# Optimization experiments

Hardware: AMD Instinct MI355X
Metric: run time of the kernel (lower is better)

Reference implementation:

```python
import jax, jax.numpy as jnp
from jax import lax
import numpy as np

B = 262144   # batch of independent series
K = 64       # forecast horizon (init k)
D_IN = 200   # Non_AR_net input dim (Linear(200,100))
H = 100      # hidden width


def setup_inputs() -> dict:
    key = jax.random.key(0)
    ks = jax.random.split(key, 10)
    f32 = jnp.float32
    x = jax.random.normal(ks[0], (B, D_IN), f32)
    last_mu = jax.random.normal(ks[1], (B,), f32)
    # last_sigma is the variance state; keep it strictly positive
    last_sigma = jax.random.uniform(ks[2], (B,), f32) + 0.5
    # MLP params (Kaiming-ish scale)
    W1 = jax.random.normal(ks[3], (D_IN, H), f32) / np.float32(np.sqrt(D_IN))
    b1 = jnp.zeros((H,), f32)
    W2 = jax.random.normal(ks[4], (H, H), f32) / np.float32(np.sqrt(H))
    b2 = jnp.zeros((H,), f32)
    W3 = jax.random.normal(ks[5], (H, K), f32) / np.float32(np.sqrt(H))
    b3 = jnp.zeros((K,), f32)
    return {
        "x": x, "last_mu": last_mu, "last_sigma": last_sigma,
        "alpha_mu": jnp.asarray(0.1, f32), "alpha_sigma": jnp.asarray(0.1, f32),
        "beta_mu": jnp.asarray(0.9, f32), "beta_sigma": jnp.asarray(0.85, f32),
        "omega_mu": jnp.asarray(0.0, f32), "omega_sigma": jnp.asarray(0.05, f32),
        "nu": jnp.asarray(5.0, f32), "norm_strength": jnp.asarray(1.0, f32),
        "W1": W1, "b1": b1, "W2": W2, "b2": b2, "W3": W3, "b3": b3,
    }


def _mlp(x, W1, b1, W2, b2, W3, b3):
    h = jax.nn.relu(x @ W1 + b1)
    h = jax.nn.relu(h @ W2 + b2)
    return h @ W3 + b3  # [B, K]


def _ar_gas(deep_preds, last_mu, last_sigma, a_mu, a_s, b_mu, b_s, o_mu, o_s, nu, ns):
    """Student-t score-driven (GAS) k-step recurrence, vectorized over batch.
    deep_preds: [B, K]; state mu, sigma2: [B]."""
    w = 1.0 + 1.0 / nu

    def step(carry, y):  # y: [B]
        mu, s2 = carry
        e = y - mu
        denom = 1.0 + e * e / (nu * s2)
        mu_new = o_mu + ns * a_mu * (w * e / denom) + b_mu * mu
        s2_new = o_s + ns * a_s * (w * e * e / denom - s2) + b_s * s2
        return (mu_new, s2_new), (mu_new, s2_new)

    (_, _), (mus, s2s) = lax.scan(step, (last_mu, last_sigma), deep_preds.T)
    return mus.T, jnp.sqrt(s2s.T)  # [B, K] each


def reference(x, last_mu, last_sigma, alpha_mu, alpha_sigma, beta_mu, beta_sigma,
              omega_mu, omega_sigma, nu, norm_strength,
              W1, b1, W2, b2, W3, b3):
    deep_preds = _mlp(x, W1, b1, W2, b2, W3, b3)            # [B, K]
    dp = lax.stop_gradient(deep_preds)                       # .detach() in torch
    mu_pred, sigma_pred = _ar_gas(dp, last_mu, last_sigma,
                                  alpha_mu, alpha_sigma, beta_mu, beta_sigma,
                                  omega_mu, omega_sigma, nu, norm_strength)
    return deep_preds * sigma_pred + mu_pred                 # [B, K]
```

## Files before the change

### kernel.cpp

```cpp
#include <hip/hip_runtime.h>
#include <hip/hip_bf16.h>

typedef short v8s __attribute__((ext_vector_type(8)));
typedef float v4f __attribute__((ext_vector_type(4)));

#define THREADS 512
#define BMROWS  128
#define W1F     0
#define W2F     49
#define W3F     77
#define W1LDS   28
#define SLABB   28672
#define LDS_TOTAL 78848

__device__ __forceinline__ unsigned short f2bf(float f) {
    union { __hip_bfloat16 h; unsigned short u; } c;
    c.h = __float2bfloat16(f);
    return c.u;
}
__device__ __forceinline__ unsigned pk2(float a, float b) {
    return (unsigned)f2bf(a) | ((unsigned)f2bf(b) << 16);
}
__device__ __forceinline__ v4f mfma16(v8s a, v8s b, v4f c) {
    return __builtin_amdgcn_mfma_f32_16x16x32_bf16(a, b, c, 0, 0, 0);
}
__device__ __forceinline__ v8s mkfrag(float4 a, float4 b) {
    union { unsigned u[4]; v8s s; } t;
    t.u[0] = pk2(a.x, a.y); t.u[1] = pk2(a.z, a.w);
    t.u[2] = pk2(b.x, b.y); t.u[3] = pk2(b.z, b.w);
    return t.s;
}
__device__ __forceinline__ void gload_lds16(const void* g, void* l) {
    __builtin_amdgcn_global_load_lds(
        (const __attribute__((address_space(1))) void*)g,
        (__attribute__((address_space(3))) void*)l, 16, 0, 0);
}

__global__ void prep_weights(const float* __restrict__ W1,
                             const float* __restrict__ W2,
                             const float* __restrict__ W3,
                             uint4* __restrict__ wf) {
    const int bid = blockIdx.x, l = threadIdx.x;
    const float* W; int K, N, KC, base, f;
    if (bid < 49)      { W = W1; K = 200; N = 100; KC = 7; base = W1F * 64; f = bid; }
    else if (bid < 77) { W = W2; K = 100; N = 100; KC = 4; base = W2F * 64; f = bid - 49; }
    else               { W = W3; K = 100; N = 64;  KC = 4; base = W3F * 64; f = bid - 77; }
    const int kc = f % KC;
    const int n  = (f / KC) * 16 + (l & 15);
    unsigned u[4];
    #pragma unroll
    for (int p = 0; p < 4; ++p) {
        const int k0 = kc * 32 + (l >> 4) * 8 + p * 2;
        const float a = (k0     < K && n < N) ? W[(size_t)k0 * N + n]       : 0.f;
        const float b = (k0 + 1 < K && n < N) ? W[(size_t)(k0 + 1) * N + n] : 0.f;
        u[p] = pk2(a, b);
    }
    wf[base + f * 64 + l] = make_uint4(u[0], u[1], u[2], u[3]);
}

__device__ __forceinline__ int sladdr(int wid, int row, int byte) {
    return SLABB + (wid << 12) + (row << 8) +
           ((((byte >> 4) ^ row) & 15) << 4) + (byte & 15);
}

__global__ __launch_bounds__(THREADS, 4)
void ar_gas_v11(const float* __restrict__ x,
                const float* __restrict__ last_mu,
                const float* __restrict__ last_sigma,
                const float* __restrict__ p_amu, const float* __restrict__ p_as,
                const float* __restrict__ p_bmu, const float* __restrict__ p_bs,
                const float* __restrict__ p_omu, const float* __restrict__ p_os,
                const float* __restrict__ p_nu,  const float* __restrict__ p_ns,
                const float* __restrict__ b1, const float* __restrict__ b2,
                const float* __restrict__ b3,
                const uint4* __restrict__ wf,
                float* __restrict__ out)
{
    extern __shared__ __align__(16) unsigned char L[];
    const int tid  = threadIdx.x;
    const int lane = tid & 63;
    const int wid  = tid >> 6;
    const int l15  = lane & 15;
    const int l4   = lane >> 4;
    const int blk  = blockIdx.x;

    const size_t gw = (size_t)blk * BMROWS + (size_t)wid * 16;
    const float* xp0 = x + (gw + l15) * 200;

    const float mu_init = last_mu[gw + l15];
    const float s2_init = last_sigma[gw + l15];

#define XLOAD(d0, d1, kk)                                               \
    { int kb = (kk) * 32 + l4 * 8;                                      \
      kb = (kb + 8 <= 200) ? kb : 168;                                  \
      d0 = *(const float4*)(xp0 + kb);                                  \
      d1 = *(const float4*)(xp0 + kb + 4); }

    float4 xv[3][2];
    XLOAD(xv[0][0], xv[0][1], 0);
    XLOAD(xv[1][0], xv[1][1], 1);
    XLOAD(xv[2][0], xv[2][1], 2);

    float bv[7];
    #pragma unroll
    for (int nt = 0; nt < 7; ++nt) {
        const int c = nt * 16 + l15;
        bv[nt] = (c < 100) ? b1[c] : 0.f;
    }

    for (int s = wid; s < 77; s += 8) {
        const int src = (s < 28) ? (W2F + s - 0) : (W1F + s - 28);
        gload_lds16(wf + src * 64 + lane, L + s * 1024);
    }
    __syncthreads();

#define FRAG(slot) (*(const uint4*)(&L[(slot) * 1024 + lane * 16]))

    v4f acc[7];
    #pragma unroll
    for (int nt = 0; nt < 7; ++nt) acc[nt] = (v4f){0.f, 0.f, 0.f, 0.f};

    #pragma unroll
    for (int kc = 0; kc < 7; ++kc) {
        uint4 bu[7];
        #pragma unroll
        for (int nt = 0; nt < 7; ++nt) bu[nt] = FRAG(W1LDS + nt * 7 + kc);
        const v8s af = mkfrag(xv[kc % 3][0], xv[kc % 3][1]);
        if (kc < 4) XLOAD(xv[kc % 3][0], xv[kc % 3][1], kc + 3);
        #pragma unroll
        for (int nt = 0; nt < 7; ++nt)
            acc[nt] = mfma16(af, *(const v8s*)&bu[nt], acc[nt]);
    }
#undef XLOAD

    __syncthreads();

    #pragma unroll
    for (int nt = 0; nt < 7; ++nt) {
        #pragma unroll
        for (int r = 0; r < 4; ++r) {
            const int row = l4 * 4 + r;
            const int c   = nt * 16 + l15;
            const float v = fmaxf(acc[nt][r] + bv[nt], 0.f);
            *(unsigned short*)(&L[sladdr(wid, row, c * 2)]) = f2bf(v);
        }
    }
    if (lane < 32)
        *(uint4*)(&L[sladdr(wid, lane >> 1, 224 + (lane & 1) * 16)]) =
            make_uint4(0, 0, 0, 0);

    float bv2[7];
    #pragma unroll
    for (int nt = 0; nt < 7; ++nt) {
        const int c = nt * 16 + l15;
        bv2[nt] = (c < 100) ? b2[c] : 0.f;
    }
    v4f acc2[7];
    #pragma unroll
    for (int nt = 0; nt < 7; ++nt) acc2[nt] = (v4f){0.f, 0.f, 0.f, 0.f};

    #pragma unroll
    for (int kc = 0; kc < 4; ++kc) {
        uint4 bu[7];
        #pragma unroll
        for (int nt = 0; nt < 7; ++nt) bu[nt] = FRAG(nt * 4 + kc);
        uint4 t0 = *(const uint4*)(&L[sladdr(wid, l15, kc * 64 + l4 * 16)]);
        const v8s af = *(v8s*)&t0;
        #pragma unroll
        for (int nt = 0; nt < 7; ++nt)
            acc2[nt] = mfma16(af, *(const v8s*)&bu[nt], acc2[nt]);
    }

    __syncthreads();

    for (int s = wid; s < 16; s += 8)
        gload_lds16(wf + (W3F + s) * 64 + lane, L + s * 1024);

    #pragma unroll
    for (int nt = 0; nt < 7; ++nt) {
        #pragma unroll
        for (int r = 0; r < 4; ++r) {
            const int row = l4 * 4 + r;
            const int c   = nt * 16 + l15;
            const float v = fmaxf(acc2[nt][r] + bv2[nt], 0.f);
            *(unsigned short*)(&L[sladdr(wid, row, c * 2)]) = f2bf(v);
        }
    }

    __syncthreads();

    float bv3[4];
    #pragma unroll
    for (int nt = 0; nt < 4; ++nt) bv3[nt] = b3[nt * 16 + l15];
    v4f acc3[4];
    #pragma unroll
    for (int nt = 0; nt < 4; ++nt) acc3[nt] = (v4f){0.f, 0.f, 0.f, 0.f};

    #pragma unroll
    for (int kc = 0; kc < 4; ++kc) {
        uint4 bu[4];
        #pragma unroll
        for (int nt = 0; nt < 4; ++nt) bu[nt] = FRAG(nt * 4 + kc);
        uint4 t0 = *(const uint4*)(&L[sladdr(wid, l15, kc * 64 + l4 * 16)]);
        const v8s af = *(v8s*)&t0;
        #pragma unroll
        for (int nt = 0; nt < 4; ++nt)
            acc3[nt] = mfma16(af, *(const v8s*)&bu[nt], acc3[nt]);
    }
#undef FRAG

    #pragma unroll
    for (int nt = 0; nt < 4; ++nt) {
        #pragma unroll
        for (int r = 0; r < 4; ++r) {
            const int row = l4 * 4 + r;
            const int c   = nt * 16 + l15;
            *(float*)(&L[sladdr(wid, row, c * 4)]) = acc3[nt][r] + bv3[nt];
        }
    }

    if (lane < 16) {
        float mu = mu_init;
        float s2 = s2_init;
        const float anu = *p_nu,  ans = *p_ns;
        const float aMu = *p_amu, aSg = *p_as;
        const float bMu = *p_bmu, bSg = *p_bs;
        const float oMu = *p_omu, oSg = *p_os;
        const float w   = 1.f + __builtin_amdgcn_rcpf(anu);
        const float cmu = ans * aMu * w;
        const float cs  = ans * aSg * w;
        const float bs2 = bSg - ans * aSg;

#define GAS_STEP(Y, O)                                                  \
        {   const float e    = (Y) - mu;                                \
            const float nus2 = anu * s2;                                \
            const float den  = fmaf(e, e, nus2);                        \
            const float r0   = __builtin_amdgcn_rcpf(den);              \
            const float p    = e * nus2 * r0;                           \
            mu = fmaf(cmu, p, fmaf(bMu, mu, oMu));                      \
            s2 = fmaf(cs, e * p, fmaf(bs2, s2, oSg));                   \
            (O) = fmaf((Y), __builtin_amdgcn_sqrtf(s2), mu); }

        #pragma unroll
        for (int q = 0; q < 16; ++q) {
            float4 d = *(float4*)(&L[sladdr(wid, lane, q * 16)]);
            float o0, o1, o2, o3;
            GAS_STEP(d.x, o0); GAS_STEP(d.y, o1);
            GAS_STEP(d.z, o2); GAS_STEP(d.w, o3);
            *(float4*)(&L[sladdr(wid, lane, q * 16)]) = make_float4(o0, o1, o2, o3);
        }
#undef GAS_STEP
    }

    #pragma unroll
    for (int i = 0; i < 4; ++i) {
        const int fi  = i * 64 + lane;
        const int row = fi >> 4, q = fi & 15;
        float4 v = *(float4*)(&L[sladdr(wid, row, q * 16)]);
        ((float4*)out)[gw * 16 + fi] = v;
    }
}

extern "C" void kernel_launch(void* const* d_in, const int* in_sizes, int n_in,
                              void* d_out, int out_size, void* d_ws, size_t ws_size,
                              hipStream_t stream) {
    const float* x          = (const float*)d_in[0];
    const float* last_mu    = (const float*)d_in[1];
    const float* last_sigma = (const float*)d_in[2];
    const float* amu        = (const float*)d_in[3];
    const float* asig       = (const float*)d_in[4];
    const float* bmu        = (const float*)d_in[5];
    const float* bsig       = (const float*)d_in[6];
    const float* omu        = (const float*)d_in[7];
    const float* osig       = (const float*)d_in[8];
    const float* nu         = (const float*)d_in[9];
    const float* ns         = (const float*)d_in[10];
    const float* W1         = (const float*)d_in[11];
    const float* b1         = (const float*)d_in[12];
    const float* W2         = (const float*)d_in[13];
    const float* b2         = (const float*)d_in[14];
    const float* W3         = (const float*)d_in[15];
    const float* b3         = (const float*)d_in[16];
    float* out = (float*)d_out;

    uint4* wf = (uint4*)d_ws;
    prep_weights<<<93, 64, 0, stream>>>(W1, W2, W3, wf);

    hipFuncSetAttribute((const void*)ar_gas_v11,
                        hipFuncAttributeMaxDynamicSharedMemorySize, LDS_TOTAL);

    const int B = in_sizes[1];
    dim3 grid(B / BMROWS), block(THREADS);
    ar_gas_v11<<<grid, block, LDS_TOTAL, stream>>>(
        x, last_mu, last_sigma,
        amu, asig, bmu, bsig, omu, osig, nu, ns,
        b1, b2, b3, wf, out);
}
```

Measured before the change: 87.08 us.

## Make kernel persistent with all weights resident in LDS and prefetched x tiles

Switches to a persistent grid of 256 blocks of 1024 threads, each looping over 4 tiles of 256 rows. All three weight matrices are loaded into LDS once per block rather than once per 128-row block, and the per-tile __syncthreads are dropped because each wave uses its own slab. The x fragments for the next tile are prefetched before the GAS recurrence runs. The cost is about 160KB of LDS per block, which allows only one block per CU, and a grid size hardcoded to B=262144.

```diff
diff --git a/kernel.cpp b/kernel.cpp
--- a/kernel.cpp
+++ b/kernel.cpp
@@ -4,14 +4,14 @@
 typedef short v8s __attribute__((ext_vector_type(8)));
 typedef float v4f __attribute__((ext_vector_type(4)));
 
-#define THREADS 512
-#define BMROWS  128
+#define THREADS 1024
+#define NBLOCKS 256
+#define NTILES  4
 #define W1F     0
 #define W2F     49
 #define W3F     77
-#define W1LDS   28
-#define SLABB   28672
-#define LDS_TOTAL 78848
+#define SLABB   95232
+#define LDS_TOTAL (95232 + 16 * 4096)
 
 __device__ __forceinline__ unsigned short f2bf(float f) {
     union { __hip_bfloat16 h; unsigned short u; } c;
@@ -64,7 +64,7 @@
 }
 
 __global__ __launch_bounds__(THREADS, 4)
-void ar_gas_v11(const float* __restrict__ x,
+void ar_gas_v15(const float* __restrict__ x,
                 const float* __restrict__ last_mu,
                 const float* __restrict__ last_sigma,
                 const float* __restrict__ p_amu, const float* __restrict__ p_as,
@@ -84,181 +84,187 @@
     const int l4   = lane >> 4;
     const int blk  = blockIdx.x;
 
-    const size_t gw = (size_t)blk * BMROWS + (size_t)wid * 16;
-    const float* xp0 = x + (gw + l15) * 200;
-
-    const float mu_init = last_mu[gw + l15];
-    const float s2_init = last_sigma[gw + l15];
-
-#define XLOAD(d0, d1, kk)                                               \
+    const float anu = *p_nu,  ans = *p_ns;
+    const float aMu = *p_amu, aSg = *p_as;
+    const float bMu = *p_bmu, bSg = *p_bs;
+    const float oMu = *p_omu, oSg = *p_os;
+    const float wS  = 1.f + __builtin_amdgcn_rcpf(anu);
+    const float cmu = ans * aMu * wS;
+    const float cs  = ans * aSg * wS;
+    const float bs2 = bSg - ans * aSg;
+
+#define XLOAD(d0, d1, xp, kk)                                           \
     { int kb = (kk) * 32 + l4 * 8;                                      \
       kb = (kb + 8 <= 200) ? kb : 168;                                  \
-      d0 = *(const float4*)(xp0 + kb);                                  \
-      d1 = *(const float4*)(xp0 + kb + 4); }
-
+      d0 = *(const float4*)((xp) + kb);                                 \
+      d1 = *(const float4*)((xp) + kb + 4); }
+
+    size_t gw = (size_t)blk * (NTILES * 256) + (size_t)wid * 16;
     float4 xv[3][2];
-    XLOAD(xv[0][0], xv[0][1], 0);
-    XLOAD(xv[1][0], xv[1][1], 1);
-    XLOAD(xv[2][0], xv[2][1], 2);
-
-    float bv[7];
-    #pragma unroll
-    for (int nt = 0; nt < 7; ++nt) {
-        const int c = nt * 16 + l15;
-        bv[nt] = (c < 100) ? b1[c] : 0.f;
+    {
+        const float* xp = x + (gw + l15) * 200;
+        XLOAD(xv[0][0], xv[0][1], xp, 0);
+        XLOAD(xv[1][0], xv[1][1], xp, 1);
+        XLOAD(xv[2][0], xv[2][1], xp, 2);
     }
 
-    for (int s = wid; s < 77; s += 8) {
-        const int src = (s < 28) ? (W2F + s - 0) : (W1F + s - 28);
-        gload_lds16(wf + src * 64 + lane, L + s * 1024);
-    }
+    for (int s = wid; s < 93; s += 16)
+        gload_lds16(wf + s * 64 + lane, L + s * 1024);
     __syncthreads();
 
 #define FRAG(slot) (*(const uint4*)(&L[(slot) * 1024 + lane * 16]))
 
-    v4f acc[7];
-    #pragma unroll
-    for (int nt = 0; nt < 7; ++nt) acc[nt] = (v4f){0.f, 0.f, 0.f, 0.f};
-
-    #pragma unroll
-    for (int kc = 0; kc < 7; ++kc) {
-        uint4 bu[7];
-        #pragma unroll
-        for (int nt = 0; nt < 7; ++nt) bu[nt] = FRAG(W1LDS + nt * 7 + kc);
-        const v8s af = mkfrag(xv[kc % 3][0], xv[kc % 3][1]);
-        if (kc < 4) XLOAD(xv[kc % 3][0], xv[kc % 3][1], kc + 3);
-        #pragma unroll
-        for (int nt = 0; nt < 7; ++nt)
-            acc[nt] = mfma16(af, *(const v8s*)&bu[nt], acc[nt]);
-    }
-#undef XLOAD
-
-    __syncthreads();
-
-    #pragma unroll
-    for (int nt = 0; nt < 7; ++nt) {
-        #pragma unroll
-        for (int r = 0; r < 4; ++r) {
-            const int row = l4 * 4 + r;
-            const int c   = nt * 16 + l15;
-            const float v = fmaxf(acc[nt][r] + bv[nt], 0.f);
-            *(unsigned short*)(&L[sladdr(wid, row, c * 2)]) = f2bf(v);
-        }
-    }
-    if (lane < 32)
-        *(uint4*)(&L[sladdr(wid, lane >> 1, 224 + (lane & 1) * 16)]) =
-            make_uint4(0, 0, 0, 0);
-
-    float bv2[7];
-    #pragma unroll
-    for (int nt = 0; nt < 7; ++nt) {
-        const int c = nt * 16 + l15;
-        bv2[nt] = (c < 100) ? b2[c] : 0.f;
-    }
-    v4f acc2[7];
-    #pragma unroll
-    for (int nt = 0; nt < 7; ++nt) acc2[nt] = (v4f){0.f, 0.f, 0.f, 0.f};
-
-    #pragma unroll
-    for (int kc = 0; kc < 4; ++kc) {
-        uint4 bu[7];
-        #pragma unroll
-        for (int nt = 0; nt < 7; ++nt) bu[nt] = FRAG(nt * 4 + kc);
-        uint4 t0 = *(const uint4*)(&L[sladdr(wid, l15, kc * 64 + l4 * 16)]);
-        const v8s af = *(v8s*)&t0;
-        #pragma unroll
-        for (int nt = 0; nt < 7; ++nt)
-            acc2[nt] = mfma16(af, *(const v8s*)&bu[nt], acc2[nt]);
-    }
-
-    __syncthreads();
-
-    for (int s = wid; s < 16; s += 8)
-        gload_lds16(wf + (W3F + s) * 64 + lane, L + s * 1024);
-
-    #pragma unroll
-    for (int nt = 0; nt < 7; ++nt) {
-        #pragma unroll
-        for (int r = 0; r < 4; ++r) {
-            const int row = l4 * 4 + r;
-            const int c   = nt * 16 + l15;
-            const float v = fmaxf(acc2[nt][r] + bv2[nt], 0.f);
-            *(unsigned short*)(&L[sladdr(wid, row, c * 2)]) = f2bf(v);
-        }
-    }
-
-    __syncthreads();
-
-    float bv3[4];
-    #pragma unroll
-    for (int nt = 0; nt < 4; ++nt) bv3[nt] = b3[nt * 16 + l15];
-    v4f acc3[4];
-    #pragma unroll
-    for (int nt = 0; nt < 4; ++nt) acc3[nt] = (v4f){0.f, 0.f, 0.f, 0.f};
-
-    #pragma unroll
-    for (int kc = 0; kc < 4; ++kc) {
-        uint4 bu[4];
-        #pragma unroll
-        for (int nt = 0; nt < 4; ++nt) bu[nt] = FRAG(nt * 4 + kc);
-        uint4 t0 = *(const uint4*)(&L[sladdr(wid, l15, kc * 64 + l4 * 16)]);
-        const v8s af = *(v8s*)&t0;
-        #pragma unroll
-        for (int nt = 0; nt < 4; ++nt)
-            acc3[nt] = mfma16(af, *(const v8s*)&bu[nt], acc3[nt]);
+    #pragma unroll 1
+    for (int t = 0; t < NTILES; ++t) {
+        const float* xp = x + (gw + l15) * 200;
+
+        const float mu_init = last_mu[gw + l15];
+        const float s2_init = last_sigma[gw + l15];
+
+        v4f acc[7];
+        #pragma unroll
+        for (int nt = 0; nt < 7; ++nt) acc[nt] = (v4f){0.f, 0.f, 0.f, 0.f};
+
+        #pragma unroll
+        for (int kc = 0; kc < 7; ++kc) {
+            uint4 bu[7];
+            #pragma unroll
+            for (int nt = 0; nt < 7; ++nt) bu[nt] = FRAG(W1F + nt * 7 + kc);
+            const v8s af = mkfrag(xv[kc % 3][0], xv[kc % 3][1]);
+            if (kc < 4) XLOAD(xv[kc % 3][0], xv[kc % 3][1], xp, kc + 3);
+            #pragma unroll
+            for (int nt = 0; nt < 7; ++nt)
+                acc[nt] = mfma16(af, *(const v8s*)&bu[nt], acc[nt]);
+        }
+
+        {
+            float bv[7];
+            #pragma unroll
+            for (int nt = 0; nt < 7; ++nt) {
+                const int c = nt * 16 + l15;
+                bv[nt] = (c < 100) ? b1[c] : 0.f;
+            }
+            #pragma unroll
+            for (int nt = 0; nt < 7; ++nt) {
+                #pragma unroll
+                for (int r = 0; r < 4; ++r) {
+                    const int row = l4 * 4 + r;
+                    const int c   = nt * 16 + l15;
+                    const float v = fmaxf(acc[nt][r] + bv[nt], 0.f);
+                    *(unsigned short*)(&L[sladdr(wid, row, c * 2)]) = f2bf(v);
+                }
+            }
+        }
+        if (lane < 32)
+            *(uint4*)(&L[sladdr(wid, lane >> 1, 224 + (lane & 1) * 16)]) =
+                make_uint4(0, 0, 0, 0);
+
+        v4f acc2[7];
+        #pragma unroll
+        for (int nt = 0; nt < 7; ++nt) acc2[nt] = (v4f){0.f, 0.f, 0.f, 0.f};
+        #pragma unroll
+        for (int kc = 0; kc < 4; ++kc) {
+            uint4 bu[7];
+            #pragma unroll
+            for (int nt = 0; nt < 7; ++nt) bu[nt] = FRAG(W2F + nt * 4 + kc);
+            uint4 t0 = *(const uint4*)(&L[sladdr(wid, l15, kc * 64 + l4 * 16)]);
+            const v8s af = *(v8s*)&t0;
+            #pragma unroll
+            for (int nt = 0; nt < 7; ++nt)
+                acc2[nt] = mfma16(af, *(const v8s*)&bu[nt], acc2[nt]);
+        }
+        {
+            float bv[7];
+            #pragma unroll
+            for (int nt = 0; nt < 7; ++nt) {
+                const int c = nt * 16 + l15;
+                bv[nt] = (c < 100) ? b2[c] : 0.f;
+            }
+            #pragma unroll
+            for (int nt = 0; nt < 7; ++nt) {
+                #pragma unroll
+                for (int r = 0; r < 4; ++r) {
+                    const int row = l4 * 4 + r;
+                    const int c   = nt * 16 + l15;
+                    const float v = fmaxf(acc2[nt][r] + bv[nt], 0.f);
+                    *(unsigned short*)(&L[sladdr(wid, row, c * 2)]) = f2bf(v);
+                }
+            }
+        }
+
+        v4f acc3[4];
+        #pragma unroll
+        for (int nt = 0; nt < 4; ++nt) acc3[nt] = (v4f){0.f, 0.f, 0.f, 0.f};
+        #pragma unroll
+        for (int kc = 0; kc < 4; ++kc) {
+            uint4 bu[4];
+            #pragma unroll
+            for (int nt = 0; nt < 4; ++nt) bu[nt] = FRAG(W3F + nt * 4 + kc);
+            uint4 t0 = *(const uint4*)(&L[sladdr(wid, l15, kc * 64 + l4 * 16)]);
+            const v8s af = *(v8s*)&t0;
+            #pragma unroll
+            for (int nt = 0; nt < 4; ++nt)
+                acc3[nt] = mfma16(af, *(const v8s*)&bu[nt], acc3[nt]);
+        }
+        {
+            float bv[4];
+            #pragma unroll
+            for (int nt = 0; nt < 4; ++nt) bv[nt] = b3[nt * 16 + l15];
+            #pragma unroll
+            for (int nt = 0; nt < 4; ++nt) {
+                #pragma unroll
+                for (int r = 0; r < 4; ++r) {
+                    const int row = l4 * 4 + r;
+                    const int c   = nt * 16 + l15;
+                    *(float*)(&L[sladdr(wid, row, c * 4)]) = acc3[nt][r] + bv[nt];
+                }
+            }
+        }
+
+        const size_t gw_next = gw + 256;
+        if (t < NTILES - 1) {
+            const float* np = x + (gw_next + l15) * 200;
+            XLOAD(xv[0][0], xv[0][1], np, 0);
+            XLOAD(xv[1][0], xv[1][1], np, 1);
+            XLOAD(xv[2][0], xv[2][1], np, 2);
+        }
+
+        if (lane < 16) {
+            float mu = mu_init;
+            float s2 = s2_init;
+#define GAS_STEP(Y, O)                                                  \
+            {   const float e    = (Y) - mu;                            \
+                const float nus2 = anu * s2;                            \
+                const float den  = fmaf(e, e, nus2);                    \
+                const float r0   = __builtin_amdgcn_rcpf(den);          \
+                const float p    = e * nus2 * r0;                       \
+                mu = fmaf(cmu, p, fmaf(bMu, mu, oMu));                  \
+                s2 = fmaf(cs, e * p, fmaf(bs2, s2, oSg));               \
+                (O) = fmaf((Y), __builtin_amdgcn_sqrtf(s2), mu); }
+            #pragma unroll
+            for (int q = 0; q < 16; ++q) {
+                float4 d = *(float4*)(&L[sladdr(wid, lane, q * 16)]);
+                float o0, o1, o2, o3;
+                GAS_STEP(d.x, o0); GAS_STEP(d.y, o1);
+                GAS_STEP(d.z, o2); GAS_STEP(d.w, o3);
+                *(float4*)(&L[sladdr(wid, lane, q * 16)]) =
+                    make_float4(o0, o1, o2, o3);
+            }
+#undef GAS_STEP
+        }
+
+        #pragma unroll
+        for (int i = 0; i < 4; ++i) {
+            const int fi  = i * 64 + lane;
+            const int row = fi >> 4, q = fi & 15;
+            float4 v = *(float4*)(&L[sladdr(wid, row, q * 16)]);
+            ((float4*)out)[gw * 16 + fi] = v;
+        }
+
+        gw = gw_next;
     }
 #undef FRAG
-
-    #pragma unroll
-    for (int nt = 0; nt < 4; ++nt) {
-        #pragma unroll
-        for (int r = 0; r < 4; ++r) {
-            const int row = l4 * 4 + r;
-            const int c   = nt * 16 + l15;
-            *(float*)(&L[sladdr(wid, row, c * 4)]) = acc3[nt][r] + bv3[nt];
-        }
-    }
-
-    if (lane < 16) {
-        float mu = mu_init;
-        float s2 = s2_init;
-        const float anu = *p_nu,  ans = *p_ns;
-        const float aMu = *p_amu, aSg = *p_as;
-        const float bMu = *p_bmu, bSg = *p_bs;
-        const float oMu = *p_omu, oSg = *p_os;
-        const float w   = 1.f + __builtin_amdgcn_rcpf(anu);
-        const float cmu = ans * aMu * w;
-        const float cs  = ans * aSg * w;
-        const float bs2 = bSg - ans * aSg;
-
-#define GAS_STEP(Y, O)                                                  \
-        {   const float e    = (Y) - mu;                                \
-            const float nus2 = anu * s2;                                \
-            const float den  = fmaf(e, e, nus2);                        \
-            const float r0   = __builtin_amdgcn_rcpf(den);              \
-            const float p    = e * nus2 * r0;                           \
-            mu = fmaf(cmu, p, fmaf(bMu, mu, oMu));                      \
-            s2 = fmaf(cs, e * p, fmaf(bs2, s2, oSg));                   \
-            (O) = fmaf((Y), __builtin_amdgcn_sqrtf(s2), mu); }
-
-        #pragma unroll
-        for (int q = 0; q < 16; ++q) {
-            float4 d = *(float4*)(&L[sladdr(wid, lane, q * 16)]);
-            float o0, o1, o2, o3;
-            GAS_STEP(d.x, o0); GAS_STEP(d.y, o1);
-            GAS_STEP(d.z, o2); GAS_STEP(d.w, o3);
-            *(float4*)(&L[sladdr(wid, lane, q * 16)]) = make_float4(o0, o1, o2, o3);
-        }
-#undef GAS_STEP
-    }
-
-    #pragma unroll
-    for (int i = 0; i < 4; ++i) {
-        const int fi  = i * 64 + lane;
-        const int row = fi >> 4, q = fi & 15;
-        float4 v = *(float4*)(&L[sladdr(wid, row, q * 16)]);
-        ((float4*)out)[gw * 16 + fi] = v;
-    }
+#undef XLOAD
 }
 
 extern "C" void kernel_launch(void* const* d_in, const int* in_sizes, int n_in,
@@ -286,12 +292,11 @@
     uint4* wf = (uint4*)d_ws;
     prep_weights<<<93, 64, 0, stream>>>(W1, W2, W3, wf);
 
-    hipFuncSetAttribute((const void*)ar_gas_v11,
+    hipFuncSetAttribute((const void*)ar_gas_v15,
                         hipFuncAttributeMaxDynamicSharedMemorySize, LDS_TOTAL);
 
-    const int B = in_sizes[1];
-    dim3 grid(B / BMROWS), block(THREADS);
-    ar_gas_v11<<<grid, block, LDS_TOTAL, stream>>>(
+    dim3 grid(NBLOCKS), block(THREADS);
+    ar_gas_v15<<<grid, block, LDS_TOTAL, stream>>>(
         x, last_mu, last_sigma,
         amu, asig, bmu, bsig, omu, osig, nu, ns,
         b1, b2, b3, wf, out);
```

After: 140.7 us. +61.6%, slower.

## Rework LDS layout with padded slabs, prefetch all x, relax launch bounds

Applied to the files above, without the earlier changes.

Replaces the XOR-swizzled per-wave activation slabs with padded-stride slabs that share LDS with the W1 fragments. Also gives W2 and W3 their own regions, so the W3 fragments can be fetched right after layer 1 and one barrier is removed. All seven x chunks are now loaded into registers up front instead of through a 3-deep rotating buffer. Launch bounds drop from 4 to 2 blocks per CU, which lets each thread use more registers but may reduce occupancy. The padded stride may bring back some LDS bank conflicts that the swizzle used to avoid.

```diff
diff --git a/kernel.cpp b/kernel.cpp
--- a/kernel.cpp
+++ b/kernel.cpp
@@ -5,13 +5,16 @@
 typedef float v4f __attribute__((ext_vector_type(4)));
 
 #define THREADS 512
+#define WAVES   8
 #define BMROWS  128
 #define W1F     0
 #define W2F     49
 #define W3F     77
-#define W1LDS   28
-#define SLABB   28672
-#define LDS_TOTAL 78848
+#define W3B     33792
+#define W2B     50176
+#define SLAB_STRIDE 264
+#define SLAB_SIZE   4224
+#define LDS_TOTAL   78848
 
 __device__ __forceinline__ unsigned short f2bf(float f) {
     union { __hip_bfloat16 h; unsigned short u; } c;
@@ -58,13 +61,8 @@
     wf[base + f * 64 + l] = make_uint4(u[0], u[1], u[2], u[3]);
 }
 
-__device__ __forceinline__ int sladdr(int wid, int row, int byte) {
-    return SLABB + (wid << 12) + (row << 8) +
-           ((((byte >> 4) ^ row) & 15) << 4) + (byte & 15);
-}
-
-__global__ __launch_bounds__(THREADS, 4)
-void ar_gas_v11(const float* __restrict__ x,
+__global__ __launch_bounds__(THREADS, 2)
+void ar_gas_v17(const float* __restrict__ x,
                 const float* __restrict__ last_mu,
                 const float* __restrict__ last_sigma,
                 const float* __restrict__ p_amu, const float* __restrict__ p_as,
@@ -85,36 +83,36 @@
     const int blk  = blockIdx.x;
 
     const size_t gw = (size_t)blk * BMROWS + (size_t)wid * 16;
-    const float* xp0 = x + (gw + l15) * 200;
-
+    const float* xp = x + (gw + l15) * 200;
+
+    float4 xv[7][2];
+    #pragma unroll
+    for (int kc = 0; kc < 7; ++kc) {
+        int kb = kc * 32 + l4 * 8;
+        kb = (kb + 8 <= 200) ? kb : 168;
+        xv[kc][0] = *(const float4*)(xp + kb);
+        xv[kc][1] = *(const float4*)(xp + kb + 4);
+    }
     const float mu_init = last_mu[gw + l15];
     const float s2_init = last_sigma[gw + l15];
 
-#define XLOAD(d0, d1, kk)                                               \
-    { int kb = (kk) * 32 + l4 * 8;                                      \
-      kb = (kb + 8 <= 200) ? kb : 168;                                  \
-      d0 = *(const float4*)(xp0 + kb);                                  \
-      d1 = *(const float4*)(xp0 + kb + 4); }
-
-    float4 xv[3][2];
-    XLOAD(xv[0][0], xv[0][1], 0);
-    XLOAD(xv[1][0], xv[1][1], 1);
-    XLOAD(xv[2][0], xv[2][1], 2);
-
-    float bv[7];
-    #pragma unroll
-    for (int nt = 0; nt < 7; ++nt) {
-        const int c = nt * 16 + l15;
-        bv[nt] = (c < 100) ? b1[c] : 0.f;
-    }
-
-    for (int s = wid; s < 77; s += 8) {
-        const int src = (s < 28) ? (W2F + s - 0) : (W1F + s - 28);
-        gload_lds16(wf + src * 64 + lane, L + s * 1024);
+    for (int s = wid; s < 77; s += WAVES) {
+        unsigned char* dst = (s < 49) ? (L + s * 1024)
+                                      : (L + W2B + (s - 49) * 1024);
+        gload_lds16(wf + s * 64 + lane, dst);
     }
     __syncthreads();
 
-#define FRAG(slot) (*(const uint4*)(&L[(slot) * 1024 + lane * 16]))
+#define FRAG_W1(f)  (*(const uint4*)(&L[(f) * 1024 + lane * 16]))
+#define FRAG_W2(f)  (*(const uint4*)(&L[W2B + (f) * 1024 + lane * 16]))
+#define FRAG_W3(f)  (*(const uint4*)(&L[W3B + (f) * 1024 + lane * 16]))
+
+    const int sb      = wid * SLAB_SIZE;
+    const int sb_epi  = sb + (l4 * 4) * SLAB_STRIDE + l15 * 2;
+    const int sb_rd   = sb + l15 * SLAB_STRIDE + l4 * 16;
+    const int sb_dpw  = sb + (l4 * 4) * SLAB_STRIDE + l15 * 4;
+    const int sb_gas  = sb + l15 * SLAB_STRIDE;
+    const int sb_st   = sb + l4 * SLAB_STRIDE + l15 * 16;
 
     v4f acc[7];
     #pragma unroll
@@ -124,99 +122,93 @@
     for (int kc = 0; kc < 7; ++kc) {
         uint4 bu[7];
         #pragma unroll
-        for (int nt = 0; nt < 7; ++nt) bu[nt] = FRAG(W1LDS + nt * 7 + kc);
-        const v8s af = mkfrag(xv[kc % 3][0], xv[kc % 3][1]);
-        if (kc < 4) XLOAD(xv[kc % 3][0], xv[kc % 3][1], kc + 3);
+        for (int nt = 0; nt < 7; ++nt) bu[nt] = FRAG_W1(nt * 7 + kc);
+        const v8s af = mkfrag(xv[kc][0], xv[kc][1]);
         #pragma unroll
         for (int nt = 0; nt < 7; ++nt)
             acc[nt] = mfma16(af, *(const v8s*)&bu[nt], acc[nt]);
     }
-#undef XLOAD
 
     __syncthreads();
 
-    #pragma unroll
-    for (int nt = 0; nt < 7; ++nt) {
-        #pragma unroll
-        for (int r = 0; r < 4; ++r) {
-            const int row = l4 * 4 + r;
-            const int c   = nt * 16 + l15;
-            const float v = fmaxf(acc[nt][r] + bv[nt], 0.f);
-            *(unsigned short*)(&L[sladdr(wid, row, c * 2)]) = f2bf(v);
+    for (int s = wid; s < 16; s += WAVES)
+        gload_lds16(wf + (W3F + s) * 64 + lane, L + W3B + s * 1024);
+
+    {
+        float bv[7];
+        #pragma unroll
+        for (int nt = 0; nt < 7; ++nt) {
+            const int c = nt * 16 + l15;
+            bv[nt] = (c < 100) ? b1[c] : 0.f;
         }
+        #pragma unroll
+        for (int nt = 0; nt < 7; ++nt)
+            #pragma unroll
+            for (int r = 0; r < 4; ++r) {
+                const float v = fmaxf(acc[nt][r] + bv[nt], 0.f);
+                *(unsigned short*)(&L[sb_epi + r * SLAB_STRIDE + nt * 32]) = f2bf(v);
+            }
     }
     if (lane < 32)
-        *(uint4*)(&L[sladdr(wid, lane >> 1, 224 + (lane & 1) * 16)]) =
+        *(uint4*)(&L[sb + (lane >> 1) * SLAB_STRIDE + 224 + (lane & 1) * 16]) =
             make_uint4(0, 0, 0, 0);
 
-    float bv2[7];
-    #pragma unroll
-    for (int nt = 0; nt < 7; ++nt) {
-        const int c = nt * 16 + l15;
-        bv2[nt] = (c < 100) ? b2[c] : 0.f;
-    }
     v4f acc2[7];
     #pragma unroll
     for (int nt = 0; nt < 7; ++nt) acc2[nt] = (v4f){0.f, 0.f, 0.f, 0.f};
-
     #pragma unroll
     for (int kc = 0; kc < 4; ++kc) {
         uint4 bu[7];
         #pragma unroll
-        for (int nt = 0; nt < 7; ++nt) bu[nt] = FRAG(nt * 4 + kc);
-        uint4 t0 = *(const uint4*)(&L[sladdr(wid, l15, kc * 64 + l4 * 16)]);
+        for (int nt = 0; nt < 7; ++nt) bu[nt] = FRAG_W2(nt * 4 + kc);
+        uint4 t0 = *(const uint4*)(&L[sb_rd + kc * 64]);
         const v8s af = *(v8s*)&t0;
         #pragma unroll
         for (int nt = 0; nt < 7; ++nt)
             acc2[nt] = mfma16(af, *(const v8s*)&bu[nt], acc2[nt]);
     }
+    {
+        float bv[7];
+        #pragma unroll
+        for (int nt = 0; nt < 7; ++nt) {
+            const int c = nt * 16 + l15;
+            bv[nt] = (c < 100) ? b2[c] : 0.f;
+        }
+        #pragma unroll
+        for (int nt = 0; nt < 7; ++nt)
+            #pragma unroll
+            for (int r = 0; r < 4; ++r) {
+                const float v = fmaxf(acc2[nt][r] + bv[nt], 0.f);
+                *(unsigned short*)(&L[sb_epi + r * SLAB_STRIDE + nt * 32]) = f2bf(v);
+            }
+    }
 
     __syncthreads();
 
-    for (int s = wid; s < 16; s += 8)
-        gload_lds16(wf + (W3F + s) * 64 + lane, L + s * 1024);
-
-    #pragma unroll
-    for (int nt = 0; nt < 7; ++nt) {
-        #pragma unroll
-        for (int r = 0; r < 4; ++r) {
-            const int row = l4 * 4 + r;
-            const int c   = nt * 16 + l15;
-            const float v = fmaxf(acc2[nt][r] + bv2[nt], 0.f);
-            *(unsigned short*)(&L[sladdr(wid, row, c * 2)]) = f2bf(v);
-        }
-    }
-
-    __syncthreads();
-
-    float bv3[4];
-    #pragma unroll
-    for (int nt = 0; nt < 4; ++nt) bv3[nt] = b3[nt * 16 + l15];
     v4f acc3[4];
     #pragma unroll
     for (int nt = 0; nt < 4; ++nt) acc3[nt] = (v4f){0.f, 0.f, 0.f, 0.f};
-
     #pragma unroll
     for (int kc = 0; kc < 4; ++kc) {
         uint4 bu[4];
         #pragma unroll
-        for (int nt = 0; nt < 4; ++nt) bu[nt] = FRAG(nt * 4 + kc);
-        uint4 t0 = *(const uint4*)(&L[sladdr(wid, l15, kc * 64 + l4 * 16)]);
+        for (int nt = 0; nt < 4; ++nt) bu[nt] = FRAG_W3(nt * 4 + kc);
+        uint4 t0 = *(const uint4*)(&L[sb_rd + kc * 64]);
         const v8s af = *(v8s*)&t0;
         #pragma unroll
         for (int nt = 0; nt < 4; ++nt)
             acc3[nt] = mfma16(af, *(const v8s*)&bu[nt], acc3[nt]);
     }
-#undef FRAG
-
-    #pragma unroll
-    for (int nt = 0; nt < 4; ++nt) {
-        #pragma unroll
-        for (int r = 0; r < 4; ++r) {
-            const int row = l4 * 4 + r;
-            const int c   = nt * 16 + l15;
-            *(float*)(&L[sladdr(wid, row, c * 4)]) = acc3[nt][r] + bv3[nt];
-        }
+    {
+        float bv[4];
+        #pragma unroll
+        for (int nt = 0; nt < 4; ++nt) bv[nt] = b3[nt * 16 + l15];
+        #pragma unroll
+        for (int nt = 0; nt < 4; ++nt)
+            #pragma unroll
+            for (int r = 0; r < 4; ++r)
+                *(float*)(&L[sb_dpw + r * SLAB_STRIDE + nt * 64]) =
+                    acc3[nt][r] + bv[nt];
     }
 
     if (lane < 16) {
@@ -243,22 +235,23 @@
 
         #pragma unroll
         for (int q = 0; q < 16; ++q) {
-            float4 d = *(float4*)(&L[sladdr(wid, lane, q * 16)]);
+            float4 d = *(float4*)(&L[sb_gas + q * 16]);
             float o0, o1, o2, o3;
             GAS_STEP(d.x, o0); GAS_STEP(d.y, o1);
             GAS_STEP(d.z, o2); GAS_STEP(d.w, o3);
-            *(float4*)(&L[sladdr(wid, lane, q * 16)]) = make_float4(o0, o1, o2, o3);
+            *(float4*)(&L[sb_gas + q * 16]) = make_float4(o0, o1, o2, o3);
         }
 #undef GAS_STEP
     }
 
     #pragma unroll
     for (int i = 0; i < 4; ++i) {
-        const int fi  = i * 64 + lane;
-        const int row = fi >> 4, q = fi & 15;
-        float4 v = *(float4*)(&L[sladdr(wid, row, q * 16)]);
-        ((float4*)out)[gw * 16 + fi] = v;
-    }
+        float4 v = *(float4*)(&L[sb_st + i * (4 * SLAB_STRIDE)]);
+        ((float4*)out)[gw * 16 + i * 64 + lane] = v;
+    }
+#undef FRAG_W1
+#undef FRAG_W2
+#undef FRAG_W3
 }
 
 extern "C" void kernel_launch(void* const* d_in, const int* in_sizes, int n_in,
@@ -286,12 +279,12 @@
     uint4* wf = (uint4*)d_ws;
     prep_weights<<<93, 64, 0, stream>>>(W1, W2, W3, wf);
 
-    hipFuncSetAttribute((const void*)ar_gas_v11,
+    hipFuncSetAttribute((const void*)ar_gas_v17,
                         hipFuncAttributeMaxDynamicSharedMemorySize, LDS_TOTAL);
 
     const int B = in_sizes[1];
     dim3 grid(B / BMROWS), block(THREADS);
-    ar_gas_v11<<<grid, block, LDS_TOTAL, stream>>>(
+    ar_gas_v17<<<grid, block, LDS_TOTAL, stream>>>(
         x, last_mu, last_sigma,
         amu, asig, bmu, bsig, omu, osig, nu, ns,
         b1, b2, b3, wf, out);
```

Result: faster. 83.32 us (-4.3%).
